# Performance work log

Hardware: AMD Instinct MI355X
Metric: run time of the kernel (lower is better)

The kernel has to match this reference:

```python
import jax, jax.numpy as jnp
import numpy as np

B, N, E, D, H = 1, 100000, 3200000, 16, 128
EPS = 1e-5


def _layer_norm(x, g, b):
    m = jnp.mean(x, axis=-1, keepdims=True)
    v = jnp.mean((x - m) ** 2, axis=-1, keepdims=True)
    return (x - m) * jax.lax.rsqrt(v + EPS) * g + b


def setup_inputs() -> dict:
    key = jax.random.key(0)
    ks = jax.random.split(key, 12)
    inp = {
        "nodes": jax.random.normal(ks[0], (B, N, D), dtype=jnp.float32),
        "edges": jax.random.randint(ks[1], (B, E, 2), 0, N, dtype=jnp.int32),
        "edge_weights": jax.random.uniform(ks[2], (B, E), dtype=jnp.float32),
    }
    dims = [(3 * D, H), (H, H), (H, H), (H, D)]
    for i, (din, dout) in enumerate(dims, start=1):
        inp[f"W{i}"] = jax.random.normal(ks[2 + i], (din, dout), dtype=jnp.float32) * (1.0 / np.sqrt(din))
        inp[f"b{i}"] = jnp.zeros((dout,), dtype=jnp.float32)
        inp[f"g{i}"] = jnp.ones((dout,), dtype=jnp.float32)
        inp[f"be{i}"] = jnp.zeros((dout,), dtype=jnp.float32)
    return inp


def reference(nodes, edges, edge_weights,
              W1, b1, g1, be1, W2, b2, g2, be2,
              W3, b3, g3, be3, W4, b4, g4, be4):
    src = edges[..., 0]  # [B,E]
    dst = edges[..., 1]
    w = edge_weights[..., None]  # [B,E,1]
    # edge-weighted endpoint features
    msg_in = jnp.take_along_axis(nodes, src[..., None], axis=1) * w   # [B,E,D]
    msg_out = jnp.take_along_axis(nodes, dst[..., None], axis=1) * w  # [B,E,D]
    # per-node sum aggregation (scatter-add over edge lists)
    b_idx = jnp.arange(B)[:, None]
    agg_in = jnp.zeros_like(nodes).at[b_idx, dst].add(msg_in)   # in-edges of node i
    agg_out = jnp.zeros_like(nodes).at[b_idx, src].add(msg_out)  # out-edges of node i
    x = jnp.concatenate([agg_in, agg_out, nodes], axis=2)  # [B,N,3D]
    x = jnp.tanh(_layer_norm(x @ W1 + b1, g1, be1))
    x = jnp.tanh(_layer_norm(x @ W2 + b2, g2, be2))
    x = jnp.tanh(_layer_norm(x @ W3 + b3, g3, be3))
    x = jnp.tanh(_layer_norm(x @ W4 + b4, g4, be4))
    return x
```

## Files before the change

kernel.cpp:

```cpp
#include <hip/hip_runtime.h>
#include <stdint.h>

#define DIM 16
#define HID 128
#define TN  64
#define ROWF 132
#define EPSF 1e-5f

__device__ __forceinline__ float safe_tanh(float x) {
    float a = fabsf(x);
    float e = __expf(2.0f * a);
    float t = 1.0f - 2.0f / (e + 1.0f);
    return copysignf(t, x);
}

__global__ void __launch_bounds__(256) edge_scatter_kernel(
    const float* __restrict__ nodes, const int* __restrict__ edges,
    const float* __restrict__ ew, float* __restrict__ agg_in,
    float* __restrict__ agg_out, int nEdges)
{
    int gid = blockIdx.x * 256 + threadIdx.x;
    int e = gid >> 4;
    if (e >= nEdges) return;
    int c = gid & 15;
    int src = edges[2 * e];
    int dst = edges[2 * e + 1];
    float w  = ew[e];
    float vs = nodes[src * DIM + c];
    float vd = nodes[dst * DIM + c];
    atomicAdd(&agg_in[dst * DIM + c], vs * w);
    atomicAdd(&agg_out[src * DIM + c], vd * w);
}

template<int K>
__device__ __forceinline__ void dense_ln_tanh(
    const float* __restrict__ W, const float* __restrict__ bias,
    const float* __restrict__ g, const float* __restrict__ be,
    float (&X)[TN][ROWF], int tid)
{
    const int c0 = (tid & 31) * 4;
    const int n0 = (tid >> 5) * 8;
    float acc[8][4];
    {
        float4 bv = *(const float4*)(bias + c0);
        #pragma unroll
        for (int i = 0; i < 8; ++i) {
            acc[i][0] = bv.x; acc[i][1] = bv.y; acc[i][2] = bv.z; acc[i][3] = bv.w;
        }
    }

    #pragma unroll 2
    for (int k = 0; k < K; k += 4) {
        float xr[8][4];
        #pragma unroll
        for (int i = 0; i < 8; ++i) {
            float4 t = *(const float4*)&X[n0 + i][k];
            xr[i][0] = t.x; xr[i][1] = t.y; xr[i][2] = t.z; xr[i][3] = t.w;
        }
        float w[4][4];
        #pragma unroll
        for (int kk = 0; kk < 4; ++kk) {
            float4 t = *(const float4*)(W + (k + kk) * HID + c0);
            w[kk][0] = t.x; w[kk][1] = t.y; w[kk][2] = t.z; w[kk][3] = t.w;
        }
        #pragma unroll
        for (int kk = 0; kk < 4; ++kk)
            #pragma unroll
            for (int i = 0; i < 8; ++i)
                #pragma unroll
                for (int j = 0; j < 4; ++j) acc[i][j] += xr[i][kk] * w[kk][j];
    }

    float s[8], q[8];
    #pragma unroll
    for (int i = 0; i < 8; ++i) {
        s[i] = acc[i][0] + acc[i][1] + acc[i][2] + acc[i][3];
        q[i] = acc[i][0]*acc[i][0] + acc[i][1]*acc[i][1]
             + acc[i][2]*acc[i][2] + acc[i][3]*acc[i][3];
    }
    #pragma unroll
    for (int m = 1; m <= 16; m <<= 1) {
        #pragma unroll
        for (int i = 0; i < 8; ++i) {
            s[i] += __shfl_xor(s[i], m);
            q[i] += __shfl_xor(q[i], m);
        }
    }

    float4 gv  = *(const float4*)(g + c0);
    float4 bev = *(const float4*)(be + c0);
    float gr[4]  = {gv.x, gv.y, gv.z, gv.w};
    float ber[4] = {bev.x, bev.y, bev.z, bev.w};

    __syncthreads();
    #pragma unroll
    for (int i = 0; i < 8; ++i) {
        float mean = s[i] * (1.0f / HID);
        float var  = fmaxf(q[i] * (1.0f / HID) - mean * mean, 0.0f);
        float r = rsqrtf(var + EPSF);
        float o[4];
        #pragma unroll
        for (int j = 0; j < 4; ++j)
            o[j] = safe_tanh((acc[i][j] - mean) * r * gr[j] + ber[j]);
        *(float4*)&X[n0 + i][c0] = make_float4(o[0], o[1], o[2], o[3]);
    }
    __syncthreads();
}

__global__ void __launch_bounds__(256, 3) mlp_kernel(
    const float* __restrict__ agg_in, const float* __restrict__ agg_out,
    const float* __restrict__ nodes,
    const float* __restrict__ W1, const float* __restrict__ b1, const float* __restrict__ g1, const float* __restrict__ be1,
    const float* __restrict__ W2, const float* __restrict__ b2, const float* __restrict__ g2, const float* __restrict__ be2,
    const float* __restrict__ W3, const float* __restrict__ b3, const float* __restrict__ g3, const float* __restrict__ be3,
    const float* __restrict__ W4, const float* __restrict__ b4, const float* __restrict__ g4, const float* __restrict__ be4,
    float* __restrict__ out, int nNodes)
{
    __shared__ float X[TN][ROWF];

    const int tid = threadIdx.x;
    const int node0 = blockIdx.x * TN;

    for (int i = tid; i < TN * 12; i += 256) {
        int n = i / 12, c4 = i - n * 12;
        int gn = node0 + n;
        float4 v = make_float4(0.f, 0.f, 0.f, 0.f);
        if (gn < nNodes) {
            if (c4 < 4)      v = *(const float4*)(agg_in  + gn * DIM + c4 * 4);
            else if (c4 < 8) v = *(const float4*)(agg_out + gn * DIM + (c4 - 4) * 4);
            else             v = *(const float4*)(nodes   + gn * DIM + (c4 - 8) * 4);
        }
        *(float4*)&X[n][c4 * 4] = v;
    }
    __syncthreads();

    dense_ln_tanh<48>(W1, b1, g1, be1, X, tid);
    dense_ln_tanh<128>(W2, b2, g2, be2, X, tid);
    dense_ln_tanh<128>(W3, b3, g3, be3, X, tid);

    {
        const int c2 = tid & 15;
        const int nb = tid >> 4;
        float a[4];
        {
            float bv = b4[c2];
            #pragma unroll
            for (int t = 0; t < 4; ++t) a[t] = bv;
        }
        #pragma unroll 2
        for (int k = 0; k < HID; k += 4) {
            float w[4];
            #pragma unroll
            for (int kk = 0; kk < 4; ++kk) w[kk] = W4[(k + kk) * DIM + c2];
            #pragma unroll
            for (int t = 0; t < 4; ++t) {
                float4 x = *(const float4*)&X[nb + 16 * t][k];
                a[t] += x.x * w[0] + x.y * w[1] + x.z * w[2] + x.w * w[3];
            }
        }
        float s[4], q[4];
        #pragma unroll
        for (int t = 0; t < 4; ++t) { s[t] = a[t]; q[t] = a[t] * a[t]; }
        #pragma unroll
        for (int m = 1; m <= 8; m <<= 1) {
            #pragma unroll
            for (int t = 0; t < 4; ++t) {
                s[t] += __shfl_xor(s[t], m);
                q[t] += __shfl_xor(q[t], m);
            }
        }
        float g4v = g4[c2], be4v = be4[c2];
        #pragma unroll
        for (int t = 0; t < 4; ++t) {
            int node = node0 + nb + 16 * t;
            if (node < nNodes) {
                float mean = s[t] * (1.0f / DIM);
                float var  = fmaxf(q[t] * (1.0f / DIM) - mean * mean, 0.0f);
                float o = safe_tanh((a[t] - mean) * rsqrtf(var + EPSF) * g4v + be4v);
                out[(size_t)node * DIM + c2] = o;
            }
        }
    }
}

extern "C" void kernel_launch(void* const* d_in, const int* in_sizes, int n_in,
                              void* d_out, int out_size, void* d_ws, size_t ws_size,
                              hipStream_t stream)
{
    const float* nodes = (const float*)d_in[0];
    const int*   edges = (const int*)d_in[1];
    const float* ew    = (const float*)d_in[2];
    const float *W1 = (const float*)d_in[3],  *b1 = (const float*)d_in[4],
                *g1 = (const float*)d_in[5],  *be1 = (const float*)d_in[6];
    const float *W2 = (const float*)d_in[7],  *b2 = (const float*)d_in[8],
                *g2 = (const float*)d_in[9],  *be2 = (const float*)d_in[10];
    const float *W3 = (const float*)d_in[11], *b3 = (const float*)d_in[12],
                *g3 = (const float*)d_in[13], *be3 = (const float*)d_in[14];
    const float *W4 = (const float*)d_in[15], *b4 = (const float*)d_in[16],
                *g4 = (const float*)d_in[17], *be4 = (const float*)d_in[18];

    const int N = in_sizes[0] / DIM;
    const int E = in_sizes[2];

    float* agg_in  = (float*)d_ws;
    float* agg_out = agg_in + (size_t)N * DIM;

    hipMemsetAsync(d_ws, 0, (size_t)2 * N * DIM * sizeof(float), stream);

    long long ethreads = (long long)E * 16;
    int egrid = (int)((ethreads + 255) / 256);
    edge_scatter_kernel<<<egrid, 256, 0, stream>>>(nodes, edges, ew,
                                                   agg_in, agg_out, E);

    int mgrid = (N + TN - 1) / TN;
    mlp_kernel<<<mgrid, 256, 0, stream>>>(agg_in, agg_out, nodes,
        W1, b1, g1, be1, W2, b2, g2, be2, W3, b3, g3, be3, W4, b4, g4, be4,
        (float*)d_out, N);
}
```

Before: 576.2 us.

## Retile MLP layers to 4x8 per-thread tiles and raise occupancy

Dense layers now give each thread 4 rows by 8 columns instead of 8 by 4. This halves shared-memory X reads per FMA at the cost of twice as many weight loads per thread, and shortens the LayerNorm shuffle reduction to 16 lanes. Launch bounds go from 3 to 4 blocks per SM to push for higher occupancy, which tightens the register budget and may cause spills. The final layer is retiled to 2x2 outputs per thread with float2 stores, and tanh now uses a hardware reciprocal instead of a division.

```diff
diff --git a/kernel.cpp b/kernel.cpp
--- a/kernel.cpp
+++ b/kernel.cpp
@@ -10,8 +10,8 @@
 __device__ __forceinline__ float safe_tanh(float x) {
     float a = fabsf(x);
     float e = __expf(2.0f * a);
-    float t = 1.0f - 2.0f / (e + 1.0f);
-    return copysignf(t, x);
+    float r = __builtin_amdgcn_rcpf(e + 1.0f);
+    return copysignf(1.0f - 2.0f * r, x);
 }
 
 __global__ void __launch_bounds__(256) edge_scatter_kernel(
@@ -38,76 +38,89 @@
     const float* __restrict__ g, const float* __restrict__ be,
     float (&X)[TN][ROWF], int tid)
 {
-    const int c0 = (tid & 31) * 4;
-    const int n0 = (tid >> 5) * 8;
-    float acc[8][4];
+    const int c0 = (tid & 15) * 8;
+    const int n0 = (tid >> 4) * 4;
+    float acc[4][8];
     {
-        float4 bv = *(const float4*)(bias + c0);
-        #pragma unroll
-        for (int i = 0; i < 8; ++i) {
-            acc[i][0] = bv.x; acc[i][1] = bv.y; acc[i][2] = bv.z; acc[i][3] = bv.w;
+        float4 bA = *(const float4*)(bias + c0);
+        float4 bB = *(const float4*)(bias + c0 + 4);
+        #pragma unroll
+        for (int i = 0; i < 4; ++i) {
+            acc[i][0] = bA.x; acc[i][1] = bA.y; acc[i][2] = bA.z; acc[i][3] = bA.w;
+            acc[i][4] = bB.x; acc[i][5] = bB.y; acc[i][6] = bB.z; acc[i][7] = bB.w;
         }
     }
 
     #pragma unroll 2
     for (int k = 0; k < K; k += 4) {
-        float xr[8][4];
-        #pragma unroll
-        for (int i = 0; i < 8; ++i) {
+        float xr[4][4];
+        #pragma unroll
+        for (int i = 0; i < 4; ++i) {
             float4 t = *(const float4*)&X[n0 + i][k];
             xr[i][0] = t.x; xr[i][1] = t.y; xr[i][2] = t.z; xr[i][3] = t.w;
         }
-        float w[4][4];
+        float wA[4][4], wB[4][4];
         #pragma unroll
         for (int kk = 0; kk < 4; ++kk) {
-            float4 t = *(const float4*)(W + (k + kk) * HID + c0);
-            w[kk][0] = t.x; w[kk][1] = t.y; w[kk][2] = t.z; w[kk][3] = t.w;
+            float4 ta = *(const float4*)(W + (k + kk) * HID + c0);
+            float4 tb = *(const float4*)(W + (k + kk) * HID + c0 + 4);
+            wA[kk][0] = ta.x; wA[kk][1] = ta.y; wA[kk][2] = ta.z; wA[kk][3] = ta.w;
+            wB[kk][0] = tb.x; wB[kk][1] = tb.y; wB[kk][2] = tb.z; wB[kk][3] = tb.w;
         }
         #pragma unroll
         for (int kk = 0; kk < 4; ++kk)
             #pragma unroll
-            for (int i = 0; i < 8; ++i)
+            for (int i = 0; i < 4; ++i) {
+                float xs = xr[i][kk];
                 #pragma unroll
-                for (int j = 0; j < 4; ++j) acc[i][j] += xr[i][kk] * w[kk][j];
-    }
-
-    float s[8], q[8];
+                for (int j = 0; j < 4; ++j) {
+                    acc[i][j]     += xs * wA[kk][j];
+                    acc[i][4 + j] += xs * wB[kk][j];
+                }
+            }
+    }
+
+    float s[4], q[4];
     #pragma unroll
-    for (int i = 0; i < 8; ++i) {
-        s[i] = acc[i][0] + acc[i][1] + acc[i][2] + acc[i][3];
-        q[i] = acc[i][0]*acc[i][0] + acc[i][1]*acc[i][1]
-             + acc[i][2]*acc[i][2] + acc[i][3]*acc[i][3];
+    for (int i = 0; i < 4; ++i) {
+        float ss = 0.f, qq = 0.f;
+        #pragma unroll
+        for (int j = 0; j < 8; ++j) { ss += acc[i][j]; qq += acc[i][j] * acc[i][j]; }
+        s[i] = ss; q[i] = qq;
     }
     #pragma unroll
-    for (int m = 1; m <= 16; m <<= 1) {
-        #pragma unroll
-        for (int i = 0; i < 8; ++i) {
+    for (int m = 1; m <= 8; m <<= 1) {
+        #pragma unroll
+        for (int i = 0; i < 4; ++i) {
             s[i] += __shfl_xor(s[i], m);
             q[i] += __shfl_xor(q[i], m);
         }
     }
 
-    float4 gv  = *(const float4*)(g + c0);
-    float4 bev = *(const float4*)(be + c0);
-    float gr[4]  = {gv.x, gv.y, gv.z, gv.w};
-    float ber[4] = {bev.x, bev.y, bev.z, bev.w};
+    float4 gA  = *(const float4*)(g + c0);
+    float4 gB  = *(const float4*)(g + c0 + 4);
+    float4 eA  = *(const float4*)(be + c0);
+    float4 eB  = *(const float4*)(be + c0 + 4);
+    float gr[8]  = {gA.x, gA.y, gA.z, gA.w, gB.x, gB.y, gB.z, gB.w};
+    float ber[8] = {eA.x, eA.y, eA.z, eA.w, eB.x, eB.y, eB.z, eB.w};
 
     __syncthreads();
     #pragma unroll
-    for (int i = 0; i < 8; ++i) {
+    for (int i = 0; i < 4; ++i) {
         float mean = s[i] * (1.0f / HID);
         float var  = fmaxf(q[i] * (1.0f / HID) - mean * mean, 0.0f);
         float r = rsqrtf(var + EPSF);
-        float o[4];
-        #pragma unroll
-        for (int j = 0; j < 4; ++j)
+        float o[8];
+        #pragma unroll
+        for (int j = 0; j < 8; ++j)
             o[j] = safe_tanh((acc[i][j] - mean) * r * gr[j] + ber[j]);
-        *(float4*)&X[n0 + i][c0] = make_float4(o[0], o[1], o[2], o[3]);
+        *(float4*)&X[n0 + i][c0]     = make_float4(o[0], o[1], o[2], o[3]);
+        *(float4*)&X[n0 + i][c0 + 4] = make_float4(o[4], o[5], o[6], o[7]);
     }
     __syncthreads();
 }
 
-__global__ void __launch_bounds__(256, 3) mlp_kernel(
+__global__ void __launch_bounds__(256, 4) mlp_kernel(
     const float* __restrict__ agg_in, const float* __restrict__ agg_out,
     const float* __restrict__ nodes,
     const float* __restrict__ W1, const float* __restrict__ b1, const float* __restrict__ g1, const float* __restrict__ be1,
@@ -139,45 +152,57 @@
     dense_ln_tanh<128>(W3, b3, g3, be3, X, tid);
 
     {
-        const int c2 = tid & 15;
-        const int nb = tid >> 4;
-        float a[4];
-        {
-            float bv = b4[c2];
-            #pragma unroll
-            for (int t = 0; t < 4; ++t) a[t] = bv;
-        }
+        const int c0 = (tid & 7) * 2;
+        const int rg = tid >> 3;
+        float a[2][2];
+        a[0][0] = a[1][0] = b4[c0];
+        a[0][1] = a[1][1] = b4[c0 + 1];
         #pragma unroll 2
         for (int k = 0; k < HID; k += 4) {
-            float w[4];
-            #pragma unroll
-            for (int kk = 0; kk < 4; ++kk) w[kk] = W4[(k + kk) * DIM + c2];
-            #pragma unroll
-            for (int t = 0; t < 4; ++t) {
-                float4 x = *(const float4*)&X[nb + 16 * t][k];
-                a[t] += x.x * w[0] + x.y * w[1] + x.z * w[2] + x.w * w[3];
-            }
-        }
-        float s[4], q[4];
-        #pragma unroll
-        for (int t = 0; t < 4; ++t) { s[t] = a[t]; q[t] = a[t] * a[t]; }
-        #pragma unroll
-        for (int m = 1; m <= 8; m <<= 1) {
-            #pragma unroll
-            for (int t = 0; t < 4; ++t) {
+            float wv[4][2];
+            #pragma unroll
+            for (int kk = 0; kk < 4; ++kk) {
+                float2 wt = *(const float2*)(W4 + (k + kk) * DIM + c0);
+                wv[kk][0] = wt.x; wv[kk][1] = wt.y;
+            }
+            #pragma unroll
+            for (int t = 0; t < 2; ++t) {
+                float4 x = *(const float4*)&X[rg * 2 + t][k];
+                float xs[4] = {x.x, x.y, x.z, x.w};
+                #pragma unroll
+                for (int kk = 0; kk < 4; ++kk) {
+                    a[t][0] += xs[kk] * wv[kk][0];
+                    a[t][1] += xs[kk] * wv[kk][1];
+                }
+            }
+        }
+        float s[2], q[2];
+        #pragma unroll
+        for (int t = 0; t < 2; ++t) {
+            s[t] = a[t][0] + a[t][1];
+            q[t] = a[t][0] * a[t][0] + a[t][1] * a[t][1];
+        }
+        #pragma unroll
+        for (int m = 1; m <= 4; m <<= 1) {
+            #pragma unroll
+            for (int t = 0; t < 2; ++t) {
                 s[t] += __shfl_xor(s[t], m);
                 q[t] += __shfl_xor(q[t], m);
             }
         }
-        float g4v = g4[c2], be4v = be4[c2];
-        #pragma unroll
-        for (int t = 0; t < 4; ++t) {
-            int node = node0 + nb + 16 * t;
+        float2 gt = *(const float2*)(g4 + c0);
+        float2 et = *(const float2*)(be4 + c0);
+        #pragma unroll
+        for (int t = 0; t < 2; ++t) {
+            int node = node0 + rg * 2 + t;
             if (node < nNodes) {
                 float mean = s[t] * (1.0f / DIM);
                 float var  = fmaxf(q[t] * (1.0f / DIM) - mean * mean, 0.0f);
-                float o = safe_tanh((a[t] - mean) * rsqrtf(var + EPSF) * g4v + be4v);
-                out[(size_t)node * DIM + c2] = o;
+                float r = rsqrtf(var + EPSF);
+                float2 o;
+                o.x = safe_tanh((a[t][0] - mean) * r * gt.x + et.x);
+                o.y = safe_tanh((a[t][1] - mean) * r * gt.y + et.y);
+                *(float2*)(out + (size_t)node * DIM + c0) = o;
             }
         }
     }
```

Result: slower. 594.4 us (+3.2%).

## Replace global atomic edge scatter with bucketed binning and LDS accumulation

Applied to the files above, without the earlier changes.

Edges are first binned by destination (and by source) into buckets of 1024 nodes, with LDS staging and batched flushes into fixed-capacity global lists. A per-bucket kernel then gathers node features and accumulates them with shared-memory atomics before writing agg_in/agg_out. This replaces the original per-channel global atomics with LDS atomics plus extra list traffic. Per-bucket capacity is fixed with no overflow check, so it is only safe for near-uniform edge distributions, and the accumulation grid has only 196 blocks. safe_tanh also switches to a hardware reciprocal.

```diff
diff --git a/kernel.cpp b/kernel.cpp
--- a/kernel.cpp
+++ b/kernel.cpp
@@ -7,11 +7,124 @@
 #define ROWF 132
 #define EPSF 1e-5f
 
+#define NB    98
+#define SLOT  32
+#define THRESH 16
+#define CAP   33792
+#define NREG  (2 * NB)
+
 __device__ __forceinline__ float safe_tanh(float x) {
     float a = fabsf(x);
     float e = __expf(2.0f * a);
-    float t = 1.0f - 2.0f / (e + 1.0f);
-    return copysignf(t, x);
+    float r = __builtin_amdgcn_rcpf(e + 1.0f);
+    return copysignf(1.0f - 2.0f * r, x);
+}
+
+__global__ void init_cursors_kernel(int* __restrict__ gcur)
+{
+    int r = threadIdx.x;
+    if (r < NREG) gcur[r] = r * CAP;
+}
+
+__device__ __forceinline__ void flush_phase(
+    int thresh, int* __restrict__ cnt, int2 (*__restrict__ stage)[SLOT],
+    int* __restrict__ gcur, int2* __restrict__ list)
+{
+    const int wid = threadIdx.x >> 6, lane = threadIdx.x & 63;
+    const int bucket = (wid & 1) * 64 + lane;
+    const int dir = wid >> 1;
+    const bool valid = bucket < NB;
+    const int r = dir * NB + (valid ? bucket : 0);
+    int c = valid ? cnt[r] : 0;
+    bool f = valid && (c >= thresh);
+    int n = f ? (c < SLOT ? c : SLOT) : 0;
+    int gpos = 0;
+    if (f) { gpos = atomicAdd(&gcur[r], n); cnt[r] = 0; }
+    unsigned long long mask = __ballot(f);
+    while (mask) {
+        int sl = __ffsll(mask) - 1; mask &= mask - 1;
+        int rb = __shfl(r, sl);
+        int nn = __shfl(n, sl);
+        int gp = __shfl(gpos, sl);
+        if (lane < nn) list[gp + lane] = stage[rb][lane];
+    }
+}
+
+__global__ void __launch_bounds__(256) bin_kernel(
+    const int2* __restrict__ edges, const float* __restrict__ ew, int E,
+    int* __restrict__ gcur, int2* __restrict__ list, int nblk)
+{
+    __shared__ int2 stage[NREG][SLOT];
+    __shared__ int cnt[NREG];
+    for (int i = threadIdx.x; i < NREG; i += 256) cnt[i] = 0;
+    __syncthreads();
+
+    const int chunk = (E + nblk - 1) / nblk;
+    const int e0 = blockIdx.x * chunk;
+    const int e1 = min(e0 + chunk, E);
+
+    for (int base = e0; base < e1; base += 512) {
+        #pragma unroll
+        for (int u = 0; u < 2; ++u) {
+            int e = base + threadIdx.x + u * 256;
+            if (e < e1) {
+                int2 sd = edges[e];
+                int wb = __float_as_int(ew[e]);
+                int r0 = sd.y >> 10;
+                int2 en0 = make_int2(((sd.y & 1023) << 17) | sd.x, wb);
+                int p0 = atomicAdd(&cnt[r0], 1);
+                if (p0 < SLOT) stage[r0][p0] = en0;
+                else list[atomicAdd(&gcur[r0], 1)] = en0;
+                int r1 = NB + (sd.x >> 10);
+                int2 en1 = make_int2(((sd.x & 1023) << 17) | sd.y, wb);
+                int p1 = atomicAdd(&cnt[r1], 1);
+                if (p1 < SLOT) stage[r1][p1] = en1;
+                else list[atomicAdd(&gcur[r1], 1)] = en1;
+            }
+        }
+        __syncthreads();
+        flush_phase(THRESH, cnt, stage, gcur, list);
+        __syncthreads();
+    }
+    flush_phase(1, cnt, stage, gcur, list);
+}
+
+__global__ void __launch_bounds__(256) accum_kernel(
+    const float* __restrict__ nodes, const int2* __restrict__ list,
+    const int* __restrict__ gcur, float* __restrict__ agg_in,
+    float* __restrict__ agg_out, int N)
+{
+    __shared__ float acc[1024 * DIM];
+    const int r = blockIdx.x;
+    const int dir = (r >= NB) ? 1 : 0;
+    const int bucket = dir ? r - NB : r;
+    for (int i = threadIdx.x; i < 1024 * DIM; i += 256) acc[i] = 0.f;
+    __syncthreads();
+
+    const int base = r * CAP;
+    const int len = gcur[r] - base;
+    const int t = threadIdx.x >> 4, c = threadIdx.x & 15;
+    for (int i0 = 0; i0 < len; i0 += 64) {
+        #pragma unroll
+        for (int u = 0; u < 4; ++u) {
+            int i = i0 + u * 16 + t;
+            if (i < len) {
+                int2 en = list[base + i];
+                int other = en.x & 0x1FFFF;
+                int local = en.x >> 17;
+                float v = __int_as_float(en.y) * nodes[other * DIM + c];
+                atomicAdd(&acc[local * DIM + c], v);
+            }
+        }
+    }
+    __syncthreads();
+
+    float* __restrict__ dst = dir ? agg_out : agg_in;
+    const int node0 = bucket << 10;
+    for (int i = threadIdx.x; i < 1024 * DIM; i += 256) {
+        int node = node0 + (i >> 4);
+        if (node < N) dst[node * DIM + (i & 15)] = acc[i];
+    }
 }
 
 __global__ void __launch_bounds__(256) edge_scatter_kernel(
@@ -26,10 +139,8 @@
     int src = edges[2 * e];
     int dst = edges[2 * e + 1];
     float w  = ew[e];
-    float vs = nodes[src * DIM + c];
-    float vd = nodes[dst * DIM + c];
-    atomicAdd(&agg_in[dst * DIM + c], vs * w);
-    atomicAdd(&agg_out[src * DIM + c], vd * w);
+    atomicAdd(&agg_in[dst * DIM + c], nodes[src * DIM + c] * w);
+    atomicAdd(&agg_out[src * DIM + c], nodes[dst * DIM + c] * w);
 }
 
 template<int K>
@@ -202,15 +313,34 @@
     const int N = in_sizes[0] / DIM;
     const int E = in_sizes[2];
 
-    float* agg_in  = (float*)d_ws;
-    float* agg_out = agg_in + (size_t)N * DIM;
-
-    hipMemsetAsync(d_ws, 0, (size_t)2 * N * DIM * sizeof(float), stream);
-
-    long long ethreads = (long long)E * 16;
-    int egrid = (int)((ethreads + 255) / 256);
-    edge_scatter_kernel<<<egrid, 256, 0, stream>>>(nodes, edges, ew,
-                                                   agg_in, agg_out, E);
+    auto align256 = [](size_t x) { return (x + 255) & ~(size_t)255; };
+    size_t o = 0;
+    size_t agg_in_off  = o; o = align256(o + (size_t)N * DIM * 4);
+    size_t agg_out_off = o; o = align256(o + (size_t)N * DIM * 4);
+    size_t gcur_off    = o; o = align256(o + (size_t)NREG * 4);
+    size_t list_off    = o; o = align256(o + (size_t)NREG * CAP * 8 + 4096);
+    size_t need = o;
+
+    float* agg_in  = (float*)((char*)d_ws + agg_in_off);
+    float* agg_out = (float*)((char*)d_ws + agg_out_off);
+
+    if (ws_size >= need) {
+        int*  gcur = (int*)((char*)d_ws + gcur_off);
+        int2* list = (int2*)((char*)d_ws + list_off);
+
+        init_cursors_kernel<<<1, 256, 0, stream>>>(gcur);
+        const int nblk = 784;
+        bin_kernel<<<nblk, 256, 0, stream>>>((const int2*)edges, ew, E,
+                                             gcur, list, nblk);
+        accum_kernel<<<NREG, 256, 0, stream>>>(nodes, list, gcur,
+                                               agg_in, agg_out, N);
+    } else {
+        hipMemsetAsync(d_ws, 0, (size_t)2 * N * DIM * 4, stream);
+        long long ethreads = (long long)E * 16;
+        int egrid = (int)((ethreads + 255) / 256);
+        edge_scatter_kernel<<<egrid, 256, 0, stream>>>(nodes, edges, ew,
+                                                       agg_in, agg_out, E);
+    }
 
     int mgrid = (N + TN - 1) / TN;
     mlp_kernel<<<mgrid, 256, 0, stream>>>(agg_in, agg_out, nodes,
```

Result: slower. 1.481 ms (+157.0%).
